# Kernel optimization log

Measured on AMD Instinct MI355X. Metric: run time of the kernel, lower is better.

Reference implementation:

```python
import jax, jax.numpy as jnp
import numpy as np

EPS = 1e-06

def setup_inputs() -> dict:
    key = jax.random.key(0)
    kq, kk, kv = jax.random.split(key, 3)
    Q = jax.random.normal(kq, (2, 32, 2048, 128), dtype=jnp.float32)
    K = jax.random.normal(kk, (2, 32, 8192, 128), dtype=jnp.float32)
    V = jax.random.normal(kv, (2, 32, 8192, 128), dtype=jnp.float32)
    return {"Q": Q, "K": K, "V": V}

def _phi(x):
    # elu(x) + 1  (alpha=1)
    return jnp.where(x > 0, x + 1.0, jnp.exp(x))

def reference(Q, K, V):
    # prepare: cache KV = K_phi^T V  [B,H,d,d], Z = sum_k K_phi  [B,H,d]
    K_phi = _phi(K)                                   # [B,H,kv,d]
    KV = jnp.einsum('bhkd,bhke->bhde', K_phi, V)      # [B,H,d,d]
    Z = jnp.sum(K_phi, axis=2)                        # [B,H,d]
    # forward
    Q_phi = _phi(Q)                                   # [B,H,q,d]
    numerator = jnp.einsum('bhqd,bhde->bhqe', Q_phi, KV)   # [B,H,q,d]
    denominator = jnp.einsum('bhqd,bhd->bhq', Q_phi, Z)[..., None] + EPS
    return numerator / denominator
```

## Files before the change

### kernel.cpp

```cpp
#include <hip/hip_runtime.h>
#include <hip/hip_bf16.h>

#define BH 64
#define NKV 8192
#define NQ 2048
#define DIM 128
#define EPSV 1e-6f

typedef __attribute__((ext_vector_type(8))) short bf16x8;
typedef __attribute__((ext_vector_type(4))) float f32x4;

__device__ __forceinline__ float phi_f(float x) { return x > 0.f ? x + 1.f : __expf(x); }

__device__ __forceinline__ ushort f2bf(float f) {
  unsigned u = __builtin_bit_cast(unsigned, f);
  u += 0x7FFFu + ((u >> 16) & 1u);
  return (ushort)(u >> 16);
}
__device__ __forceinline__ float bf2f(ushort h) {
  unsigned u = ((unsigned)h) << 16;
  return __builtin_bit_cast(float, u);
}

#define KT 32
#define LDK 40

__global__ __launch_bounds__(256, 4) void k1_kv(
    const float* __restrict__ Kg, const float* __restrict__ Vg,
    ushort* __restrict__ part, float* __restrict__ zpart, int nch, int ck)
{
  __shared__ ushort ktl[DIM * LDK];
  __shared__ ushort vtl[DIM * LDK];
  __shared__ float zl[DIM];

  const int wg = blockIdx.x;
  const int bh = wg / nch;
  const int c  = wg - bh * nch;
  const int t  = threadIdx.x;
  const int lane = t & 63;
  const int w  = t >> 6;
  const int p  = t >> 4;
  const int db = (t & 15) * 8;

  const long base = (long)bh * NKV * DIM + (long)c * ck * DIM;
  const float* Kp = Kg + base;
  const float* Vp = Vg + base;

  if (t < DIM) zl[t] = 0.f;
  __syncthreads();

  f32x4 acc[8][2];
#pragma unroll
  for (int i = 0; i < 8; i++) {
    acc[i][0] = (f32x4){0.f, 0.f, 0.f, 0.f};
    acc[i][1] = (f32x4){0.f, 0.f, 0.f, 0.f};
  }
  float zacc[8];
#pragma unroll
  for (int j = 0; j < 8; j++) zacc[j] = 0.f;

  const int kk = (lane >> 4) * 8;

  for (int k0 = 0; k0 < ck; k0 += KT) {
    const float* kr = Kp + (long)(k0 + 2 * p) * DIM + db;
    float4 ka0 = *(const float4*)(kr);
    float4 ka1 = *(const float4*)(kr + 4);
    float4 kb0 = *(const float4*)(kr + DIM);
    float4 kb1 = *(const float4*)(kr + DIM + 4);
    const float* vr = Vp + (long)(k0 + 2 * p) * DIM + db;
    float4 va0 = *(const float4*)(vr);
    float4 va1 = *(const float4*)(vr + 4);
    float4 vb0 = *(const float4*)(vr + DIM);
    float4 vb1 = *(const float4*)(vr + DIM + 4);

    float k0a[8] = {ka0.x, ka0.y, ka0.z, ka0.w, ka1.x, ka1.y, ka1.z, ka1.w};
    float k1a[8] = {kb0.x, kb0.y, kb0.z, kb0.w, kb1.x, kb1.y, kb1.z, kb1.w};
    float v0a[8] = {va0.x, va0.y, va0.z, va0.w, va1.x, va1.y, va1.z, va1.w};
    float v1a[8] = {vb0.x, vb0.y, vb0.z, vb0.w, vb1.x, vb1.y, vb1.z, vb1.w};

    __syncthreads();

#pragma unroll
    for (int j = 0; j < 8; j++) {
      int row = db + j;
      int sw = ((row >> 3) & 3) << 3;
      int col = (2 * p) ^ sw;
      ushort a = f2bf(phi_f(k0a[j]));
      ushort b = f2bf(phi_f(k1a[j]));
      zacc[j] += bf2f(a) + bf2f(b);
      *(unsigned*)&ktl[row * LDK + col] = (unsigned)a | ((unsigned)b << 16);
      ushort x = f2bf(v0a[j]);
      ushort y = f2bf(v1a[j]);
      *(unsigned*)&vtl[row * LDK + col] = (unsigned)x | ((unsigned)y << 16);
    }
    __syncthreads();

    bf16x8 bfr[2];
#pragma unroll
    for (int et = 0; et < 2; et++) {
      int e = w * 32 + et * 16 + (lane & 15);
      int kk2 = kk ^ (((e >> 3) & 3) << 3);
      bfr[et] = *(const bf16x8*)&vtl[e * LDK + kk2];
    }
#pragma unroll
    for (int dt = 0; dt < 8; dt++) {
      int dd = dt * 16 + (lane & 15);
      int kk2 = kk ^ (((dd >> 3) & 3) << 3);
      bf16x8 afr = *(const bf16x8*)&ktl[dd * LDK + kk2];
      acc[dt][0] = __builtin_amdgcn_mfma_f32_16x16x32_bf16(afr, bfr[0], acc[dt][0], 0, 0, 0);
      acc[dt][1] = __builtin_amdgcn_mfma_f32_16x16x32_bf16(afr, bfr[1], acc[dt][1], 0, 0, 0);
    }
  }

  ushort* pp = part + (long)wg * (DIM * DIM);
#pragma unroll
  for (int dt = 0; dt < 8; dt++) {
    int d0 = dt * 16 + (lane >> 4) * 4;
#pragma unroll
    for (int et = 0; et < 2; et++) {
      int e = w * 32 + et * 16 + (lane & 15);
      ushort o[4];
#pragma unroll
      for (int r = 0; r < 4; r++) o[r] = f2bf(acc[dt][et][r]);
      *(uint2*)&pp[(long)e * DIM + d0] = *(uint2*)o;
    }
  }
#pragma unroll
  for (int j = 0; j < 8; j++) atomicAdd(&zl[db + j], zacc[j]);
  __syncthreads();
  if (t < DIM) zpart[(long)wg * DIM + t] = zl[t];
}

template<int NCH>
__global__ __launch_bounds__(256) void k_red(
    const ushort* __restrict__ part, const float* __restrict__ zpart,
    ushort* __restrict__ kvt, float* __restrict__ zout)
{
  const int bh = blockIdx.x >> 2;
  const int quad = blockIdx.x & 3;
  const int t = threadIdx.x;
  const long pbase = (long)bh * NCH * (DIM * DIM);

#pragma unroll
  for (int i = 0; i < 2; i++) {
    int u4 = quad * 512 + t + i * 256;
    long off = pbase + (long)u4 * 8;
    float s[8] = {0.f, 0.f, 0.f, 0.f, 0.f, 0.f, 0.f, 0.f};
#pragma unroll
    for (int cc = 0; cc < NCH; cc++) {
      uint4 v = *(const uint4*)&part[off + (long)cc * (DIM * DIM)];
      unsigned ws_[4] = {v.x, v.y, v.z, v.w};
#pragma unroll
      for (int h = 0; h < 4; h++) {
        s[2 * h]     += bf2f((ushort)(ws_[h] & 0xFFFFu));
        s[2 * h + 1] += bf2f((ushort)(ws_[h] >> 16));
      }
    }
    unsigned o[4];
#pragma unroll
    for (int h = 0; h < 4; h++)
      o[h] = (unsigned)f2bf(s[2 * h]) | ((unsigned)f2bf(s[2 * h + 1]) << 16);
    *(uint4*)&kvt[(long)bh * (DIM * DIM) + (long)u4 * 8] =
        make_uint4(o[0], o[1], o[2], o[3]);
  }

  if (quad == 0 && t < DIM) {
    float s = 0.f;
#pragma unroll
    for (int cc = 0; cc < NCH; cc++)
      s += zpart[((long)bh * NCH + cc) * DIM + t];
    zout[(long)bh * DIM + t] = s;
  }
}

#define QB 64
#define LDQ 136

__global__ __launch_bounds__(256) void k2_fwd(
    const float* __restrict__ Qg, const ushort* __restrict__ kvt,
    const float* __restrict__ zg, float* __restrict__ outg)
{
  __shared__ ushort ql[QB * LDQ];
  __shared__ ushort kvl[DIM * LDQ];
  __shared__ float zl[DIM];
  __shared__ float dpart[4][QB];
  __shared__ float invd[QB];

  const int bid = blockIdx.x;
  const int bh = bid >> 5;
  const int q0 = (bid & 31) * QB;
  const int t = threadIdx.x;
  const int lane = t & 63;
  const int w = t >> 6;

  if (t < DIM) zl[t] = zg[(long)bh * DIM + t];

  const float* Qp = Qg + ((long)bh * NQ + q0) * DIM;
#pragma unroll
  for (int i = 0; i < 8; i++) {
    int idx4 = t + i * 256;
    int row = idx4 >> 5;
    int c4 = idx4 & 31;
    float4 v = *(const float4*)(Qp + (long)row * DIM + c4 * 4);
    ushort a = f2bf(phi_f(v.x)), b = f2bf(phi_f(v.y));
    ushort cq = f2bf(phi_f(v.z)), dq = f2bf(phi_f(v.w));
    uint2 pk;
    pk.x = (unsigned)a | ((unsigned)b << 16);
    pk.y = (unsigned)cq | ((unsigned)dq << 16);
    *(uint2*)&ql[row * LDQ + c4 * 4] = pk;
  }
  const ushort* kp = kvt + (long)bh * (DIM * DIM);
#pragma unroll
  for (int i = 0; i < 8; i++) {
    int idx8 = t + i * 256;
    int row = idx8 >> 4;
    int c8 = idx8 & 15;
    uint4 vv = *(const uint4*)(kp + row * DIM + c8 * 8);
    *(uint4*)&kvl[row * LDQ + c8 * 8] = vv;
  }
  __syncthreads();

  {
    int row = t & (QB - 1);
    int q4 = t >> 6;
    float s = 0.f;
#pragma unroll
    for (int i = 0; i < 4; i++) {
      int d0 = q4 * 32 + i * 8;
      bf16x8 qv = *(const bf16x8*)&ql[row * LDQ + d0];
#pragma unroll
      for (int j = 0; j < 8; j++)
        s += bf2f((ushort)qv[j]) * zl[d0 + j];
    }
    dpart[q4][row] = s;
  }
  __syncthreads();
  if (t < QB) {
    float den = dpart[0][t] + dpart[1][t] + dpart[2][t] + dpart[3][t] + EPSV;
    invd[t] = 1.f / den;
  }
  __syncthreads();

  const int kk = (lane >> 4) * 8;
  const int qrow = w * 16 + (lane & 15);
  f32x4 acc[8];
#pragma unroll
  for (int et = 0; et < 8; et++) acc[et] = (f32x4){0.f, 0.f, 0.f, 0.f};

#pragma unroll
  for (int d0 = 0; d0 < DIM; d0 += 32) {
    bf16x8 afr = *(const bf16x8*)&ql[qrow * LDQ + d0 + kk];
#pragma unroll
    for (int et = 0; et < 8; et++) {
      int e = et * 16 + (lane & 15);
      bf16x8 bfr = *(const bf16x8*)&kvl[e * LDQ + d0 + kk];
      acc[et] = __builtin_amdgcn_mfma_f32_16x16x32_bf16(afr, bfr, acc[et], 0, 0, 0);
    }
  }

  float* op = outg + ((long)bh * NQ + q0) * DIM;
#pragma unroll
  for (int et = 0; et < 8; et++) {
    int e = et * 16 + (lane & 15);
    int r0 = w * 16 + (lane >> 4) * 4;
#pragma unroll
    for (int r = 0; r < 4; r++) {
      float val = acc[et][r] * invd[r0 + r];
      op[(long)(r0 + r) * DIM + e] = val;
    }
  }
}

extern "C" void kernel_launch(void* const* d_in, const int* in_sizes, int n_in,
                              void* d_out, int out_size, void* d_ws, size_t ws_size,
                              hipStream_t stream) {
  const float* Q  = (const float*)d_in[0];
  const float* Km = (const float*)d_in[1];
  const float* Vm = (const float*)d_in[2];
  float* out = (float*)d_out;

  char* ws = (char*)d_ws;
  ushort* kvt = (ushort*)ws;
  float* zred = (float*)(ws + (size_t)BH * DIM * DIM * 2);
  size_t fixed = (size_t)BH * DIM * DIM * 2 + (size_t)BH * DIM * 4;

  int nch = 16;
  while (nch > 1) {
    size_t need = fixed + (size_t)BH * nch * DIM * DIM * 2 + (size_t)BH * nch * DIM * 4;
    if (need <= ws_size) break;
    nch >>= 1;
  }
  ushort* partb = (ushort*)(ws + fixed);
  float* zpart = (float*)(ws + fixed + (size_t)BH * nch * DIM * DIM * 2);
  int ck = NKV / nch;

  k1_kv<<<BH * nch, 256, 0, stream>>>(Km, Vm, partb, zpart, nch, ck);

  dim3 rg(BH * 4);
  switch (nch) {
    case 16: k_red<16><<<rg, 256, 0, stream>>>(partb, zpart, kvt, zred); break;
    case 8:  k_red<8> <<<rg, 256, 0, stream>>>(partb, zpart, kvt, zred); break;
    case 4:  k_red<4> <<<rg, 256, 0, stream>>>(partb, zpart, kvt, zred); break;
    case 2:  k_red<2> <<<rg, 256, 0, stream>>>(partb, zpart, kvt, zred); break;
    default: k_red<1> <<<rg, 256, 0, stream>>>(partb, zpart, kvt, zred); break;
  }

  k2_fwd<<<BH * 32, 256, 0, stream>>>(Q, kvt, zred, out);
}
```

Measured before the change: 166.5 us.

## Software-prefetch next K/V tile in registers and split KV reduction into more chunks

The K/V prepare kernel now loads the next tile's K and V into registers while converting the current tile, so global latency overlaps with the phi/bf16 conversion and MFMA work. Launch bounds drop from 4 to 3 waves per SIMD to make room for the extra registers. The chunk count rises to 32 (if workspace allows) for more workgroups and parallelism, at the cost of a larger partial buffer and more reduction traffic in k_red.

Result: slower. 196.0 us (+17.7%).

```diff
diff --git a/kernel.cpp b/kernel.cpp
--- a/kernel.cpp
+++ b/kernel.cpp
@@ -25,7 +25,7 @@
 #define KT 32
 #define LDK 40
 
-__global__ __launch_bounds__(256, 4) void k1_kv(
+__global__ __launch_bounds__(256, 3) void k1_kv(
     const float* __restrict__ Kg, const float* __restrict__ Vg,
     ushort* __restrict__ part, float* __restrict__ zpart, int nch, int ck)
 {
@@ -43,11 +43,10 @@
   const int db = (t & 15) * 8;
 
   const long base = (long)bh * NKV * DIM + (long)c * ck * DIM;
-  const float* Kp = Kg + base;
-  const float* Vp = Vg + base;
+  const float* Kp = Kg + base + (long)(2 * p) * DIM + db;
+  const float* Vp = Vg + base + (long)(2 * p) * DIM + db;
 
   if (t < DIM) zl[t] = 0.f;
-  __syncthreads();
 
   f32x4 acc[8][2];
 #pragma unroll
@@ -61,37 +60,57 @@
 
   const int kk = (lane >> 4) * 8;
 
+  float4 st[8];
+  st[0] = *(const float4*)(Kp);
+  st[1] = *(const float4*)(Kp + 4);
+  st[2] = *(const float4*)(Kp + DIM);
+  st[3] = *(const float4*)(Kp + DIM + 4);
+  st[4] = *(const float4*)(Vp);
+  st[5] = *(const float4*)(Vp + 4);
+  st[6] = *(const float4*)(Vp + DIM);
+  st[7] = *(const float4*)(Vp + DIM + 4);
+
+  __syncthreads();
+
   for (int k0 = 0; k0 < ck; k0 += KT) {
-    const float* kr = Kp + (long)(k0 + 2 * p) * DIM + db;
-    float4 ka0 = *(const float4*)(kr);
-    float4 ka1 = *(const float4*)(kr + 4);
-    float4 kb0 = *(const float4*)(kr + DIM);
-    float4 kb1 = *(const float4*)(kr + DIM + 4);
-    const float* vr = Vp + (long)(k0 + 2 * p) * DIM + db;
-    float4 va0 = *(const float4*)(vr);
-    float4 va1 = *(const float4*)(vr + 4);
-    float4 vb0 = *(const float4*)(vr + DIM);
-    float4 vb1 = *(const float4*)(vr + DIM + 4);
-
-    float k0a[8] = {ka0.x, ka0.y, ka0.z, ka0.w, ka1.x, ka1.y, ka1.z, ka1.w};
-    float k1a[8] = {kb0.x, kb0.y, kb0.z, kb0.w, kb1.x, kb1.y, kb1.z, kb1.w};
-    float v0a[8] = {va0.x, va0.y, va0.z, va0.w, va1.x, va1.y, va1.z, va1.w};
-    float v1a[8] = {vb0.x, vb0.y, vb0.z, vb0.w, vb1.x, vb1.y, vb1.z, vb1.w};
-
-    __syncthreads();
-
+    float k0a[8] = {st[0].x, st[0].y, st[0].z, st[0].w, st[1].x, st[1].y, st[1].z, st[1].w};
+    float k1a[8] = {st[2].x, st[2].y, st[2].z, st[2].w, st[3].x, st[3].y, st[3].z, st[3].w};
+    float v0a[8] = {st[4].x, st[4].y, st[4].z, st[4].w, st[5].x, st[5].y, st[5].z, st[5].w};
+    float v1a[8] = {st[6].x, st[6].y, st[6].z, st[6].w, st[7].x, st[7].y, st[7].z, st[7].w};
+
+    unsigned pkK[8], pkV[8];
 #pragma unroll
     for (int j = 0; j < 8; j++) {
-      int row = db + j;
-      int sw = ((row >> 3) & 3) << 3;
-      int col = (2 * p) ^ sw;
       ushort a = f2bf(phi_f(k0a[j]));
       ushort b = f2bf(phi_f(k1a[j]));
       zacc[j] += bf2f(a) + bf2f(b);
-      *(unsigned*)&ktl[row * LDK + col] = (unsigned)a | ((unsigned)b << 16);
+      pkK[j] = (unsigned)a | ((unsigned)b << 16);
       ushort x = f2bf(v0a[j]);
       ushort y = f2bf(v1a[j]);
-      *(unsigned*)&vtl[row * LDK + col] = (unsigned)x | ((unsigned)y << 16);
+      pkV[j] = (unsigned)x | ((unsigned)y << 16);
+    }
+
+    if (k0 + KT < ck) {
+      const float* kr = Kp + (long)(k0 + KT) * DIM;
+      const float* vr = Vp + (long)(k0 + KT) * DIM;
+      st[0] = *(const float4*)(kr);
+      st[1] = *(const float4*)(kr + 4);
+      st[2] = *(const float4*)(kr + DIM);
+      st[3] = *(const float4*)(kr + DIM + 4);
+      st[4] = *(const float4*)(vr);
+      st[5] = *(const float4*)(vr + 4);
+      st[6] = *(const float4*)(vr + DIM);
+      st[7] = *(const float4*)(vr + DIM + 4);
+    }
+
+    __syncthreads();
+
+#pragma unroll
+    for (int j = 0; j < 8; j++) {
+      int row = db + j;
+      int col = (2 * p) ^ (((row >> 3) & 3) << 3);
+      *(unsigned*)&ktl[row * LDK + col] = pkK[j];
+      *(unsigned*)&vtl[row * LDK + col] = pkV[j];
     }
     __syncthreads();
 
@@ -284,7 +303,7 @@
   float* zred = (float*)(ws + (size_t)BH * DIM * DIM * 2);
   size_t fixed = (size_t)BH * DIM * DIM * 2 + (size_t)BH * DIM * 4;
 
-  int nch = 16;
+  int nch = 32;
   while (nch > 1) {
     size_t need = fixed + (size_t)BH * nch * DIM * DIM * 2 + (size_t)BH * nch * DIM * 4;
     if (need <= ws_size) break;
@@ -298,6 +317,7 @@
 
   dim3 rg(BH * 4);
   switch (nch) {
+    case 32: k_red<32><<<rg, 256, 0, stream>>>(partb, zpart, kvt, zred); break;
     case 16: k_red<16><<<rg, 256, 0, stream>>>(partb, zpart, kvt, zred); break;
     case 8:  k_red<8> <<<rg, 256, 0, stream>>>(partb, zpart, kvt, zred); break;
     case 4:  k_red<4> <<<rg, 256, 0, stream>>>(partb, zpart, kvt, zred); break;
```

## Double-buffer KV accumulation tiles with 512 threads and register prefetch

Applied to the files above, without the earlier changes.

The K_phi^T V kernel moves to 512 threads per block: half load and convert K and half load V, each wave computes one 16-column e-tile instead of two. LDS tiles are double-buffered and the next tiles are prefetched into registers two iterations ahead, so each step needs one barrier instead of two and global loads overlap the MFMA work. This targets memory-latency stalls in the streaming pass over K and V, at the cost of more LDS, more threads per block and extra prefetch registers, which may lower occupancy.

Result: no change. 164.2 us (-1.4%).

```diff
diff --git a/kernel.cpp b/kernel.cpp
--- a/kernel.cpp
+++ b/kernel.cpp
@@ -25,12 +25,12 @@
 #define KT 32
 #define LDK 40
 
-__global__ __launch_bounds__(256, 4) void k1_kv(
+__global__ __launch_bounds__(512, 4) void k1_kv(
     const float* __restrict__ Kg, const float* __restrict__ Vg,
     ushort* __restrict__ part, float* __restrict__ zpart, int nch, int ck)
 {
-  __shared__ ushort ktl[DIM * LDK];
-  __shared__ ushort vtl[DIM * LDK];
+  __shared__ ushort ktl[2][DIM * LDK];
+  __shared__ ushort vtl[2][DIM * LDK];
   __shared__ float zl[DIM];
 
   const int wg = blockIdx.x;
@@ -39,94 +39,100 @@
   const int t  = threadIdx.x;
   const int lane = t & 63;
   const int w  = t >> 6;
-  const int p  = t >> 4;
-  const int db = (t & 15) * 8;
+  const int isV = t >> 8;
+  const int ts = t & 255;
+  const int p  = ts >> 4;
+  const int db = (ts & 15) * 8;
 
   const long base = (long)bh * NKV * DIM + (long)c * ck * DIM;
-  const float* Kp = Kg + base;
-  const float* Vp = Vg + base;
+  const float* Sp = (isV ? Vg : Kg) + base + (long)(2 * p) * DIM + db;
 
   if (t < DIM) zl[t] = 0.f;
-  __syncthreads();
-
-  f32x4 acc[8][2];
-#pragma unroll
-  for (int i = 0; i < 8; i++) {
-    acc[i][0] = (f32x4){0.f, 0.f, 0.f, 0.f};
-    acc[i][1] = (f32x4){0.f, 0.f, 0.f, 0.f};
-  }
+
+  f32x4 acc[8];
+#pragma unroll
+  for (int i = 0; i < 8; i++) acc[i] = (f32x4){0.f, 0.f, 0.f, 0.f};
   float zacc[8];
 #pragma unroll
   for (int j = 0; j < 8; j++) zacc[j] = 0.f;
 
   const int kk = (lane >> 4) * 8;
-
-  for (int k0 = 0; k0 < ck; k0 += KT) {
-    const float* kr = Kp + (long)(k0 + 2 * p) * DIM + db;
-    float4 ka0 = *(const float4*)(kr);
-    float4 ka1 = *(const float4*)(kr + 4);
-    float4 kb0 = *(const float4*)(kr + DIM);
-    float4 kb1 = *(const float4*)(kr + DIM + 4);
-    const float* vr = Vp + (long)(k0 + 2 * p) * DIM + db;
-    float4 va0 = *(const float4*)(vr);
-    float4 va1 = *(const float4*)(vr + 4);
-    float4 vb0 = *(const float4*)(vr + DIM);
-    float4 vb1 = *(const float4*)(vr + DIM + 4);
-
-    float k0a[8] = {ka0.x, ka0.y, ka0.z, ka0.w, ka1.x, ka1.y, ka1.z, ka1.w};
-    float k1a[8] = {kb0.x, kb0.y, kb0.z, kb0.w, kb1.x, kb1.y, kb1.z, kb1.w};
-    float v0a[8] = {va0.x, va0.y, va0.z, va0.w, va1.x, va1.y, va1.z, va1.w};
-    float v1a[8] = {vb0.x, vb0.y, vb0.z, vb0.w, vb1.x, vb1.y, vb1.z, vb1.w};
-
-    __syncthreads();
-
-#pragma unroll
-    for (int j = 0; j < 8; j++) {
-      int row = db + j;
-      int sw = ((row >> 3) & 3) << 3;
-      int col = (2 * p) ^ sw;
-      ushort a = f2bf(phi_f(k0a[j]));
-      ushort b = f2bf(phi_f(k1a[j]));
-      zacc[j] += bf2f(a) + bf2f(b);
-      *(unsigned*)&ktl[row * LDK + col] = (unsigned)a | ((unsigned)b << 16);
-      ushort x = f2bf(v0a[j]);
-      ushort y = f2bf(v1a[j]);
-      *(unsigned*)&vtl[row * LDK + col] = (unsigned)x | ((unsigned)y << 16);
-    }
-    __syncthreads();
-
-    bf16x8 bfr[2];
-#pragma unroll
-    for (int et = 0; et < 2; et++) {
-      int e = w * 32 + et * 16 + (lane & 15);
-      int kk2 = kk ^ (((e >> 3) & 3) << 3);
-      bfr[et] = *(const bf16x8*)&vtl[e * LDK + kk2];
-    }
-#pragma unroll
-    for (int dt = 0; dt < 8; dt++) {
-      int dd = dt * 16 + (lane & 15);
-      int kk2 = kk ^ (((dd >> 3) & 3) << 3);
-      bf16x8 afr = *(const bf16x8*)&ktl[dd * LDK + kk2];
-      acc[dt][0] = __builtin_amdgcn_mfma_f32_16x16x32_bf16(afr, bfr[0], acc[dt][0], 0, 0, 0);
-      acc[dt][1] = __builtin_amdgcn_mfma_f32_16x16x32_bf16(afr, bfr[1], acc[dt][1], 0, 0, 0);
-    }
+  const int e  = w * 16 + (lane & 15);
+  const int kke = kk ^ (((e >> 3) & 3) << 3);
+
+  const int ntile = ck / KT;
+
+  float4 stA[4], stB[4];
+#define LOADT(dst, ti) do {                                  \
+    const float* _s = Sp + (long)(ti) * (KT * DIM);          \
+    dst[0] = *(const float4*)(_s);                           \
+    dst[1] = *(const float4*)(_s + 4);                       \
+    dst[2] = *(const float4*)(_s + DIM);                     \
+    dst[3] = *(const float4*)(_s + DIM + 4);                 \
+  } while (0)
+
+  LOADT(stA, 0);
+  LOADT(stB, 1);
+
+#define PROC(stX, ti, bufi) do {                                           \
+    float r0[8] = {stX[0].x, stX[0].y, stX[0].z, stX[0].w,                 \
+                   stX[1].x, stX[1].y, stX[1].z, stX[1].w};                \
+    float r1[8] = {stX[2].x, stX[2].y, stX[2].z, stX[2].w,                 \
+                   stX[3].x, stX[3].y, stX[3].z, stX[3].w};                \
+    unsigned pk[8];                                                        \
+    if (isV == 0) {                                                        \
+      _Pragma("unroll")                                                    \
+      for (int j = 0; j < 8; j++) {                                        \
+        ushort a = f2bf(phi_f(r0[j]));                                     \
+        ushort b = f2bf(phi_f(r1[j]));                                     \
+        zacc[j] += bf2f(a) + bf2f(b);                                      \
+        pk[j] = (unsigned)a | ((unsigned)b << 16);                         \
+      }                                                                    \
+    } else {                                                               \
+      _Pragma("unroll")                                                    \
+      for (int j = 0; j < 8; j++) {                                        \
+        ushort a = f2bf(r0[j]);                                            \
+        ushort b = f2bf(r1[j]);                                            \
+        pk[j] = (unsigned)a | ((unsigned)b << 16);                         \
+      }                                                                    \
+    }                                                                      \
+    if ((ti) + 2 < ntile) LOADT(stX, (ti) + 2);                            \
+    ushort* dst = isV ? vtl[bufi] : ktl[bufi];                             \
+    _Pragma("unroll")                                                      \
+    for (int j = 0; j < 8; j++) {                                          \
+      int row = db + j;                                                    \
+      int col = (2 * p) ^ (((row >> 3) & 3) << 3);                         \
+      *(unsigned*)&dst[row * LDK + col] = pk[j];                           \
+    }                                                                      \
+    __syncthreads();                                                       \
+    bf16x8 bfr = *(const bf16x8*)&vtl[bufi][e * LDK + kke];                \
+    _Pragma("unroll")                                                      \
+    for (int dt = 0; dt < 8; dt++) {                                       \
+      int dd = dt * 16 + (lane & 15);                                      \
+      int kkd = kk ^ (((dd >> 3) & 3) << 3);                               \
+      bf16x8 afr = *(const bf16x8*)&ktl[bufi][dd * LDK + kkd];             \
+      acc[dt] = __builtin_amdgcn_mfma_f32_16x16x32_bf16(afr, bfr, acc[dt], 0, 0, 0); \
+    }                                                                      \
+  } while (0)
+
+  for (int ti = 0; ti < ntile; ti += 2) {
+    PROC(stA, ti, 0);
+    PROC(stB, ti + 1, 1);
   }
 
   ushort* pp = part + (long)wg * (DIM * DIM);
 #pragma unroll
   for (int dt = 0; dt < 8; dt++) {
     int d0 = dt * 16 + (lane >> 4) * 4;
-#pragma unroll
-    for (int et = 0; et < 2; et++) {
-      int e = w * 32 + et * 16 + (lane & 15);
-      ushort o[4];
-#pragma unroll
-      for (int r = 0; r < 4; r++) o[r] = f2bf(acc[dt][et][r]);
-      *(uint2*)&pp[(long)e * DIM + d0] = *(uint2*)o;
-    }
-  }
-#pragma unroll
-  for (int j = 0; j < 8; j++) atomicAdd(&zl[db + j], zacc[j]);
+    ushort o[4];
+#pragma unroll
+    for (int r = 0; r < 4; r++) o[r] = f2bf(acc[dt][r]);
+    *(uint2*)&pp[(long)e * DIM + d0] = *(uint2*)o;
+  }
+  if (isV == 0) {
+#pragma unroll
+    for (int j = 0; j < 8; j++) atomicAdd(&zl[db + j], zacc[j]);
+  }
   __syncthreads();
   if (t < DIM) zpart[(long)wg * DIM + t] = zl[t];
 }
@@ -294,7 +300,7 @@
   float* zpart = (float*)(ws + fixed + (size_t)BH * nch * DIM * DIM * 2);
   int ck = NKV / nch;
 
-  k1_kv<<<BH * nch, 256, 0, stream>>>(Km, Vm, partb, zpart, nch, ck);
+  k1_kv<<<BH * nch, 512, 0, stream>>>(Km, Vm, partb, zpart, nch, ck);
 
   dim3 rg(BH * 4);
   switch (nch) {
```
